# Optimization experiments

Measured on AMD Instinct MI355X. Metric: run time of the kernel, lower is better.

## Reference

```python
import jax, jax.numpy as jnp
import numpy as np

EPS = 1e-8  # torch CosineSimilarity default eps


def _level_loss(ts, rs, temperature):
    # ts, rs: [B, N, D] flattened child fmaps (targets / reconstructions)
    tn = ts / jnp.maximum(jnp.linalg.norm(ts, axis=-1, keepdims=True), EPS)
    rn = rs / jnp.maximum(jnp.linalg.norm(rs, axis=-1, keepdims=True), EPS)
    s_tr = jnp.einsum('bnd,bmd->bnm', tn, rn) / temperature  # cos(zi_t, zj_r)
    s_tt = jnp.einsum('bnd,bmd->bnm', tn, tn) / temperature  # cos(zi_t, zk_t)
    N = ts.shape[1]
    neg_inf = jnp.finfo(s_tt.dtype).min
    # negatives from t-t exclude k == i; t-r row i includes all j (j==i is the positive)
    s_tt_masked = jnp.where(jnp.eye(N, dtype=bool)[None], neg_inf, s_tt)
    logits = jnp.concatenate([s_tr, s_tt_masked], axis=-1)  # [B, N, 2N]
    pos = jnp.diagonal(s_tr, axis1=1, axis2=2)  # [B, N]
    # CrossEntropyLoss(sum) with label at the positive slot: -pos + logsumexp(logits)
    return jnp.sum(jax.nn.logsumexp(logits, axis=-1) - pos)


def reference(ts0, rs0, ts1, rs1, ts2, rs2, partnet_ids):
    temperature = 0.5
    batch_size = 256
    total = (_level_loss(ts0, rs0, temperature)
             + _level_loss(ts1, rs1, temperature)
             + _level_loss(ts2, rs2, temperature))
    return total / (2 * batch_size)


def setup_inputs() -> dict:
    key = jax.random.key(0)
    ks = jax.random.split(key, 7)
    B, N = 256, 16
    return {
        'ts0': jax.random.normal(ks[0], (B, N, 4096), dtype=jnp.float32),
        'rs0': jax.random.normal(ks[1], (B, N, 4096), dtype=jnp.float32),
        'ts1': jax.random.normal(ks[2], (B, N, 2048), dtype=jnp.float32),
        'rs1': jax.random.normal(ks[3], (B, N, 2048), dtype=jnp.float32),
        'ts2': jax.random.normal(ks[4], (B, N, 1024), dtype=jnp.float32),
        'rs2': jax.random.normal(ks[5], (B, N, 1024), dtype=jnp.float32),
        'partnet_ids': jax.random.randint(ks[6], (B,), 0, 1000, dtype=jnp.int64 if jax.config.jax_enable_x64 else jnp.int32),
    }
```

## Files before the change

### kernel.cpp

```cpp
#include <hip/hip_runtime.h>
#include <math.h>

#define NTX_EPS 1e-8f

typedef __fp16 half8 __attribute__((ext_vector_type(8)));
typedef __fp16 half2v __attribute__((ext_vector_type(2)));
typedef float f32x4 __attribute__((ext_vector_type(4)));

union H8 { half8 v8; half2v v2[4]; };

__device__ __forceinline__ half8 pack8(const float4& a, const float4& b) {
    H8 u;
    u.v2[0] = __builtin_amdgcn_cvt_pkrtz(a.x, a.y);
    u.v2[1] = __builtin_amdgcn_cvt_pkrtz(a.z, a.w);
    u.v2[2] = __builtin_amdgcn_cvt_pkrtz(b.x, b.y);
    u.v2[3] = __builtin_amdgcn_cvt_pkrtz(b.z, b.w);
    return u.v8;
}

__global__ __launch_bounds__(64)
void ntxent_partial(const float* __restrict__ ts0, const float* __restrict__ rs0,
                    const float* __restrict__ ts1, const float* __restrict__ rs1,
                    const float* __restrict__ ts2, const float* __restrict__ rs2,
                    float* __restrict__ ws, float* __restrict__ out)
{
    __shared__ float Gs[16][33];
    __shared__ float rn2[16];
    __shared__ float tnS[16], rnS[16];

    const int bid  = blockIdx.x;
    const int b    = bid / 7;
    const int slot = bid % 7;

    const float* tp; const float* rp; int D; int chunk0;
    if (slot < 4)      { tp = ts0; rp = rs0; D = 4096; chunk0 = slot; }
    else if (slot < 6) { tp = ts1; rp = rs1; D = 2048; chunk0 = slot - 4; }
    else               { tp = ts2; rp = rs2; D = 1024; chunk0 = 0; }

    const int l   = threadIdx.x;
    const int row = l & 15;
    const int kg  = l >> 4;

    const size_t rbase = (size_t)b * 16 * D + (size_t)row * D
                       + (size_t)chunk0 * 1024 + (size_t)kg * 8;
    const float* tsrc = tp + rbase;
    const float* rsrc = rp + rbase;

    f32x4 acc_tt = {0.f, 0.f, 0.f, 0.f};
    f32x4 acc_tr = {0.f, 0.f, 0.f, 0.f};
    f32x4 acc_rr = {0.f, 0.f, 0.f, 0.f};

    float4 ta = *(const float4*)(tsrc);
    float4 tb = *(const float4*)(tsrc + 4);
    float4 ra = *(const float4*)(rsrc);
    float4 rb = *(const float4*)(rsrc + 4);

#pragma unroll 2
    for (int s = 0; s < 32; ++s) {
        float4 nta, ntb, nra, nrb;
        if (s + 1 < 32) {
            const float* tn = tsrc + (size_t)(s + 1) * 32;
            const float* rn = rsrc + (size_t)(s + 1) * 32;
            nta = *(const float4*)(tn);
            ntb = *(const float4*)(tn + 4);
            nra = *(const float4*)(rn);
            nrb = *(const float4*)(rn + 4);
        }
        half8 tf = pack8(ta, tb);
        half8 rf = pack8(ra, rb);
        acc_tt = __builtin_amdgcn_mfma_f32_16x16x32_f16(tf, tf, acc_tt, 0, 0, 0);
        acc_tr = __builtin_amdgcn_mfma_f32_16x16x32_f16(tf, rf, acc_tr, 0, 0, 0);
        acc_rr = __builtin_amdgcn_mfma_f32_16x16x32_f16(rf, rf, acc_rr, 0, 0, 0);
        ta = nta; tb = ntb; ra = nra; rb = nrb;
    }

    const int m = row;
    if (slot != 6) {
        float* slotp = ws + (size_t)(b * 6 + slot) * 528;
#pragma unroll
        for (int r = 0; r < 4; ++r) {
            const int n = kg * 4 + r;
            slotp[n * 32 + m]      = acc_tt[r];
            slotp[n * 32 + 16 + m] = acc_tr[r];
        }
        if ((m >> 2) == kg) slotp[512 + m] = acc_rr[m & 3];
        return;
    }

#pragma unroll
    for (int r = 0; r < 4; ++r) {
        const int n = kg * 4 + r;
        Gs[n][m]      = acc_tt[r];
        Gs[n][16 + m] = acc_tr[r];
    }
    if ((m >> 2) == kg) rn2[m] = acc_rr[m & 3];
    __syncthreads();

    if (l < 16) {
        tnS[l] = fmaxf(sqrtf(Gs[l][l]), NTX_EPS);
        rnS[l] = fmaxf(sqrtf(rn2[l]), NTX_EPS);
    }
    __syncthreads();

    float loss = 0.f;
    if (l < 16) {
        const int n = l;
        const float itn = 2.0f / tnS[n];
        float lg[32];
#pragma unroll
        for (int j = 0; j < 16; ++j)
            lg[j] = Gs[n][16 + j] * itn / rnS[j];
#pragma unroll
        for (int k = 0; k < 16; ++k)
            lg[16 + k] = Gs[n][k] * itn / tnS[k];
        const float pos = lg[n];
        float mx = -3.4e38f;
#pragma unroll
        for (int j = 0; j < 32; ++j)
            mx = (j == 16 + n) ? mx : fmaxf(mx, lg[j]);
        float sm = 0.f;
#pragma unroll
        for (int j = 0; j < 32; ++j)
            sm += (j == 16 + n) ? 0.f : expf(lg[j] - mx);
        loss = logf(sm) + mx - pos;
    }
    loss += __shfl_xor(loss, 1, 64);
    loss += __shfl_xor(loss, 2, 64);
    loss += __shfl_xor(loss, 4, 64);
    loss += __shfl_xor(loss, 8, 64);
    if (l == 0) atomicAdd(out, loss * (1.0f / 512.0f));
}

__global__ __launch_bounds__(64)
void ntxent_finish(const float* __restrict__ ws, float* __restrict__ out)
{
    __shared__ float G[16][33];
    __shared__ float rn2s[16];
    __shared__ float tn[16], rn[16];

    const int bid = blockIdx.x;
    const int b   = bid >> 1;
    const int lvl = bid & 1;
    const int base = b * 6 + (lvl ? 4 : 0);
    const int cnt  = lvl ? 2 : 4;
    const int l = threadIdx.x;

    for (int e = l; e < 512; e += 64) {
        float s = 0.f;
        for (int c = 0; c < cnt; ++c) s += ws[(size_t)(base + c) * 528 + e];
        G[e >> 5][e & 31] = s;
    }
    if (l < 16) {
        float s = 0.f;
        for (int c = 0; c < cnt; ++c) s += ws[(size_t)(base + c) * 528 + 512 + l];
        rn2s[l] = s;
    }
    __syncthreads();
    if (l < 16) {
        tn[l] = fmaxf(sqrtf(G[l][l]), NTX_EPS);
        rn[l] = fmaxf(sqrtf(rn2s[l]), NTX_EPS);
    }
    __syncthreads();

    float loss = 0.f;
    if (l < 16) {
        const int n = l;
        const float itn = 2.0f / tn[n];
        float lg[32];
#pragma unroll
        for (int j = 0; j < 16; ++j)
            lg[j] = G[n][16 + j] * itn / rn[j];
#pragma unroll
        for (int k = 0; k < 16; ++k)
            lg[16 + k] = G[n][k] * itn / tn[k];
        const float pos = lg[n];
        float mx = -3.4e38f;
#pragma unroll
        for (int j = 0; j < 32; ++j)
            mx = (j == 16 + n) ? mx : fmaxf(mx, lg[j]);
        float sm = 0.f;
#pragma unroll
        for (int j = 0; j < 32; ++j)
            sm += (j == 16 + n) ? 0.f : expf(lg[j] - mx);
        loss = logf(sm) + mx - pos;
    }
    loss += __shfl_xor(loss, 1, 64);
    loss += __shfl_xor(loss, 2, 64);
    loss += __shfl_xor(loss, 4, 64);
    loss += __shfl_xor(loss, 8, 64);
    if (l == 0) atomicAdd(out, loss * (1.0f / 512.0f));
}

extern "C" void kernel_launch(void* const* d_in, const int* in_sizes, int n_in,
                              void* d_out, int out_size, void* d_ws, size_t ws_size,
                              hipStream_t stream) {
    const float* ts0 = (const float*)d_in[0];
    const float* rs0 = (const float*)d_in[1];
    const float* ts1 = (const float*)d_in[2];
    const float* rs1 = (const float*)d_in[3];
    const float* ts2 = (const float*)d_in[4];
    const float* rs2 = (const float*)d_in[5];
    float* out = (float*)d_out;
    float* ws  = (float*)d_ws;

    hipMemsetAsync(out, 0, sizeof(float), stream);

    const int B = in_sizes[0] / (16 * 4096);
    hipLaunchKernelGGL(ntxent_partial, dim3(B * 7), dim3(64), 0, stream,
                       ts0, rs0, ts1, rs1, ts2, rs2, ws, out);
    hipLaunchKernelGGL(ntxent_finish, dim3(B * 2), dim3(64), 0, stream,
                       ws, out);
}
```

Before: 65.80 us.

## Split each block's K-range across four waves with LDS reduction of Gram tiles

Each block of the partial kernel now has four wavefronts instead of one. Each wave processes a quarter of the 1024-column chunk with a double-buffered prefetch of two steps, and the per-wave MFMA accumulators are reduced through shared memory before being written out or used for the loss. The aim is more memory-level parallelism and latency hiding per block, since a single wave streaming 32 sequential steps was latency-bound. The cost is extra LDS traffic, a barrier, and larger blocks that may lower the number of resident blocks per CU.

```diff
diff --git a/kernel.cpp b/kernel.cpp
--- a/kernel.cpp
+++ b/kernel.cpp
@@ -18,15 +18,17 @@
     return u.v8;
 }
 
-__global__ __launch_bounds__(64)
+__global__ __launch_bounds__(256)
 void ntxent_partial(const float* __restrict__ ts0, const float* __restrict__ rs0,
                     const float* __restrict__ ts1, const float* __restrict__ rs1,
                     const float* __restrict__ ts2, const float* __restrict__ rs2,
                     float* __restrict__ ws, float* __restrict__ out)
 {
+    __shared__ float redTT[4][256];
+    __shared__ float redTR[4][256];
+    __shared__ float redRR[4][16];
     __shared__ float Gs[16][33];
-    __shared__ float rn2[16];
-    __shared__ float tnS[16], rnS[16];
+    __shared__ float rn2[16], tnS[16], rnS[16];
 
     const int bid  = blockIdx.x;
     const int b    = bid / 7;
@@ -37,98 +39,107 @@
     else if (slot < 6) { tp = ts1; rp = rs1; D = 2048; chunk0 = slot - 4; }
     else               { tp = ts2; rp = rs2; D = 1024; chunk0 = 0; }
 
-    const int l   = threadIdx.x;
+    const int t   = threadIdx.x;
+    const int w   = t >> 6;
+    const int l   = t & 63;
     const int row = l & 15;
     const int kg  = l >> 4;
 
-    const size_t rbase = (size_t)b * 16 * D + (size_t)row * D
-                       + (size_t)chunk0 * 1024 + (size_t)kg * 8;
-    const float* tsrc = tp + rbase;
-    const float* rsrc = rp + rbase;
+    const size_t base = (size_t)b * 16 * D + (size_t)row * D
+                      + (size_t)chunk0 * 1024 + (size_t)w * 256 + (size_t)kg * 8;
+    const float* tsrc = tp + base;
+    const float* rsrc = rp + base;
 
     f32x4 acc_tt = {0.f, 0.f, 0.f, 0.f};
     f32x4 acc_tr = {0.f, 0.f, 0.f, 0.f};
     f32x4 acc_rr = {0.f, 0.f, 0.f, 0.f};
 
-    float4 ta = *(const float4*)(tsrc);
-    float4 tb = *(const float4*)(tsrc + 4);
-    float4 ra = *(const float4*)(rsrc);
-    float4 rb = *(const float4*)(rsrc + 4);
-
-#pragma unroll 2
-    for (int s = 0; s < 32; ++s) {
-        float4 nta, ntb, nra, nrb;
-        if (s + 1 < 32) {
-            const float* tn = tsrc + (size_t)(s + 1) * 32;
-            const float* rn = rsrc + (size_t)(s + 1) * 32;
-            nta = *(const float4*)(tn);
-            ntb = *(const float4*)(tn + 4);
-            nra = *(const float4*)(rn);
-            nrb = *(const float4*)(rn + 4);
+    float4 stg[2][4];
+#pragma unroll
+    for (int p = 0; p < 2; ++p) {
+        stg[p][0] = *(const float4*)(tsrc + p * 32);
+        stg[p][1] = *(const float4*)(tsrc + p * 32 + 4);
+        stg[p][2] = *(const float4*)(rsrc + p * 32);
+        stg[p][3] = *(const float4*)(rsrc + p * 32 + 4);
+    }
+#pragma unroll
+    for (int s = 0; s < 8; ++s) {
+        half8 tf = pack8(stg[s & 1][0], stg[s & 1][1]);
+        half8 rf = pack8(stg[s & 1][2], stg[s & 1][3]);
+        if (s + 2 < 8) {
+            stg[s & 1][0] = *(const float4*)(tsrc + (s + 2) * 32);
+            stg[s & 1][1] = *(const float4*)(tsrc + (s + 2) * 32 + 4);
+            stg[s & 1][2] = *(const float4*)(rsrc + (s + 2) * 32);
+            stg[s & 1][3] = *(const float4*)(rsrc + (s + 2) * 32 + 4);
         }
-        half8 tf = pack8(ta, tb);
-        half8 rf = pack8(ra, rb);
         acc_tt = __builtin_amdgcn_mfma_f32_16x16x32_f16(tf, tf, acc_tt, 0, 0, 0);
         acc_tr = __builtin_amdgcn_mfma_f32_16x16x32_f16(tf, rf, acc_tr, 0, 0, 0);
         acc_rr = __builtin_amdgcn_mfma_f32_16x16x32_f16(rf, rf, acc_rr, 0, 0, 0);
-        ta = nta; tb = ntb; ra = nra; rb = nrb;
     }
 
     const int m = row;
+#pragma unroll
+    for (int r = 0; r < 4; ++r) {
+        const int n = kg * 4 + r;
+        redTT[w][n * 16 + m] = acc_tt[r];
+        redTR[w][n * 16 + m] = acc_tr[r];
+    }
+    if ((m >> 2) == kg) redRR[w][m] = acc_rr[m & 3];
+    __syncthreads();
+
+    const int n  = t >> 4;
+    const int mm = t & 15;
+    const float tt = redTT[0][t] + redTT[1][t] + redTT[2][t] + redTT[3][t];
+    const float tr = redTR[0][t] + redTR[1][t] + redTR[2][t] + redTR[3][t];
+
     if (slot != 6) {
         float* slotp = ws + (size_t)(b * 6 + slot) * 528;
-#pragma unroll
-        for (int r = 0; r < 4; ++r) {
-            const int n = kg * 4 + r;
-            slotp[n * 32 + m]      = acc_tt[r];
-            slotp[n * 32 + 16 + m] = acc_tr[r];
-        }
-        if ((m >> 2) == kg) slotp[512 + m] = acc_rr[m & 3];
+        slotp[n * 32 + mm]      = tt;
+        slotp[n * 32 + 16 + mm] = tr;
+        if (t < 16)
+            slotp[512 + t] = redRR[0][t] + redRR[1][t] + redRR[2][t] + redRR[3][t];
         return;
     }
 
-#pragma unroll
-    for (int r = 0; r < 4; ++r) {
-        const int n = kg * 4 + r;
-        Gs[n][m]      = acc_tt[r];
-        Gs[n][16 + m] = acc_tr[r];
-    }
-    if ((m >> 2) == kg) rn2[m] = acc_rr[m & 3];
-    __syncthreads();
-
-    if (l < 16) {
-        tnS[l] = fmaxf(sqrtf(Gs[l][l]), NTX_EPS);
-        rnS[l] = fmaxf(sqrtf(rn2[l]), NTX_EPS);
+    Gs[n][mm]      = tt;
+    Gs[n][16 + mm] = tr;
+    if (t < 16)
+        rn2[t] = redRR[0][t] + redRR[1][t] + redRR[2][t] + redRR[3][t];
+    __syncthreads();
+
+    if (t < 16) {
+        tnS[t] = fmaxf(sqrtf(Gs[t][t]), NTX_EPS);
+        rnS[t] = fmaxf(sqrtf(rn2[t]), NTX_EPS);
     }
     __syncthreads();
 
     float loss = 0.f;
-    if (l < 16) {
-        const int n = l;
-        const float itn = 2.0f / tnS[n];
+    if (t < 16) {
+        const int nn = t;
+        const float itn = 2.0f / tnS[nn];
         float lg[32];
 #pragma unroll
         for (int j = 0; j < 16; ++j)
-            lg[j] = Gs[n][16 + j] * itn / rnS[j];
+            lg[j] = Gs[nn][16 + j] * itn / rnS[j];
 #pragma unroll
         for (int k = 0; k < 16; ++k)
-            lg[16 + k] = Gs[n][k] * itn / tnS[k];
-        const float pos = lg[n];
+            lg[16 + k] = Gs[nn][k] * itn / tnS[k];
+        const float pos = lg[nn];
         float mx = -3.4e38f;
 #pragma unroll
         for (int j = 0; j < 32; ++j)
-            mx = (j == 16 + n) ? mx : fmaxf(mx, lg[j]);
+            mx = (j == 16 + nn) ? mx : fmaxf(mx, lg[j]);
         float sm = 0.f;
 #pragma unroll
         for (int j = 0; j < 32; ++j)
-            sm += (j == 16 + n) ? 0.f : expf(lg[j] - mx);
+            sm += (j == 16 + nn) ? 0.f : expf(lg[j] - mx);
         loss = logf(sm) + mx - pos;
     }
     loss += __shfl_xor(loss, 1, 64);
     loss += __shfl_xor(loss, 2, 64);
     loss += __shfl_xor(loss, 4, 64);
     loss += __shfl_xor(loss, 8, 64);
-    if (l == 0) atomicAdd(out, loss * (1.0f / 512.0f));
+    if (t == 0) atomicAdd(out, loss * (1.0f / 512.0f));
 }
 
 __global__ __launch_bounds__(64)
@@ -206,7 +217,7 @@
     hipMemsetAsync(out, 0, sizeof(float), stream);
 
     const int B = in_sizes[0] / (16 * 4096);
-    hipLaunchKernelGGL(ntxent_partial, dim3(B * 7), dim3(64), 0, stream,
+    hipLaunchKernelGGL(ntxent_partial, dim3(B * 7), dim3(256), 0, stream,
                        ts0, rs0, ts1, rs1, ts2, rs2, ws, out);
     hipLaunchKernelGGL(ntxent_finish, dim3(B * 2), dim3(64), 0, stream,
                        ws, out);
```

Result: slower. 67.96 us (+3.3%).
